# Optimization experiments

Measured on AMD Instinct MI355X. Metric: run time of the kernel, lower is better.

## Reference

```python
import jax, jax.numpy as jnp
import numpy as np
import math

B, C, H, W = 8, 64, 256, 256
E, NH = 256, 8
HD = E // NH  # 32


def get_coords(h, w):
    xx, yy = jnp.meshgrid(jnp.arange(h, dtype=jnp.float32), jnp.arange(w, dtype=jnp.float32), indexing='ij')
    return jnp.stack((xx.reshape(-1), yy.reshape(-1)), axis=-1)  # [N, 2]


def setup_inputs() -> dict:
    key = jax.random.key(0)
    ks = jax.random.split(key, 12)
    def xavier(k, shape):
        fan_out, fan_in = shape
        a = math.sqrt(6.0 / (fan_in + fan_out))
        return jax.random.uniform(k, shape, jnp.float32, -a, a)
    x = jax.random.normal(ks[0], (B, C, H, W), jnp.float32)
    z = jax.random.normal(ks[1], (B, C), jnp.float32)
    pos = jax.random.uniform(ks[2], (B, NH, 2), jnp.float32) * (H - 1)
    Wq = xavier(ks[3], (E, C)); bq = jnp.zeros((E,), jnp.float32)
    Wk = xavier(ks[4], (E, C)); bk = jnp.zeros((E,), jnp.float32)
    Wv = xavier(ks[5], (E, C)); bv = jnp.zeros((E,), jnp.float32)
    Wp = xavier(ks[6], (HD, 2)); bp = jax.random.uniform(ks[7], (HD,), jnp.float32, -1.0, 1.0) / math.sqrt(2.0)
    return {"x": x, "z": z, "pos": pos, "Wq": Wq, "bq": bq, "Wk": Wk, "bk": bk,
            "Wv": Wv, "bv": bv, "Wp": Wp, "bp": bp}


def reference(x, z, pos, Wq, bq, Wk, bk, Wv, bv, Wp, bp):
    b, c, h, w = x.shape
    n = h * w
    x_flat = x.reshape(b, c, n).transpose(0, 2, 1)          # [B, N, C]
    pos_grid = get_coords(h, w)                              # [N, 2]
    q = (z @ Wq.T + bq).reshape(b, NH, HD)                   # [B, H, hd]
    k = (x_flat @ Wk.T + bk).reshape(b, n, NH, HD)           # [B, N, H, hd]
    # relative-position modulation of keys
    rel = pos_grid[None, :, None, :] - pos[:, None, :, :]    # [B, N, H, 2]
    qxk = rel @ Wp.T + bp                                    # [B, N, H, hd]
    k = k * qxk
    v = x_flat @ Wv.T + bv                                   # [B, N, E]
    attn_logits = jnp.einsum('bhc,bnhc->bnh', q, k) / math.sqrt(HD)
    attention = jax.nn.softmax(attn_logits, axis=1)          # softmax over N
    pos_out = jnp.einsum('bnh,nx->bhx', attention, pos_grid) # [B, H, 2]
    values = jnp.einsum('bnh,bnc->bhc', attention, v)        # [B, H, E]
    return (values, pos_out)
```

## Files before the change

kernel.cpp:

```cpp
#include <hip/hip_runtime.h>

#define NN    65536
#define NSUB  128
#define NBLK  (NN/NSUB)

typedef short bf16x8 __attribute__((ext_vector_type(8)));
typedef float f32x4v __attribute__((ext_vector_type(4)));
typedef unsigned short ushort_t;
typedef unsigned int uint_t;

#define XSTR   72
#define XHI_B  0
#define XLO_B  18432
#define LGA_B  18432
#define LGSTR  28
#define PSTR   136
#define F32C_B 36864
#define RED_B  53248
#define SMEM_BYTES 53632

#define WTHI_B  0
#define WTLO_B  32768
#define CJ_B    65536
#define PM_B    66304
#define PL_B    197376
#define PSP_B   328448
#define PSX_B   590592
#define Q_B     8979200
#define QSTR    68

__device__ __forceinline__ uint_t bf16_rne_bits(float f) {
  uint_t u = __float_as_uint(f);
  return (u + 0x7FFFu + ((u >> 16) & 1u)) >> 16;
}
__device__ __forceinline__ uint_t cvt_pk_bf16(float a, float b) {
  uint_t r;
  asm("v_cvt_pk_bf16_f32 %0, %1, %2" : "=v"(r) : "v"(a), "v"(b));
  return r;
}
template <int CTRL>
__device__ __forceinline__ float dpp_add(float x) {
  int t = __builtin_amdgcn_update_dpp(0, __float_as_int(x), CTRL, 0xf, 0xf, false);
  return x + __int_as_float(t);
}
template <int CTRL>
__device__ __forceinline__ float dpp_maxs(float x) {
  int t = __builtin_amdgcn_update_dpp((int)0xFF800000u, __float_as_int(x), CTRL, 0xf, 0xf, false);
  return fmaxf(x, __int_as_float(t));
}
__device__ __forceinline__ float wave_sum(float x) {
  x = dpp_add<0x111>(x); x = dpp_add<0x112>(x); x = dpp_add<0x114>(x);
  x = dpp_add<0x118>(x); x = dpp_add<0x142>(x); x = dpp_add<0x143>(x);
  return __int_as_float(__builtin_amdgcn_readlane(__float_as_int(x), 63));
}
__device__ __forceinline__ float wave_max(float x) {
  x = dpp_maxs<0x111>(x); x = dpp_maxs<0x112>(x); x = dpp_maxs<0x114>(x);
  x = dpp_maxs<0x118>(x); x = dpp_maxs<0x142>(x); x = dpp_maxs<0x143>(x);
  return __int_as_float(__builtin_amdgcn_readlane(__float_as_int(x), 63));
}

__global__ __launch_bounds__(64) void prep_kernel(
    const float* __restrict__ z,  const float* __restrict__ Wq, const float* __restrict__ bq,
    const float* __restrict__ Wk, const float* __restrict__ bk,
    const float* __restrict__ Wp, const float* __restrict__ bp,
    ushort_t* __restrict__ WThi, ushort_t* __restrict__ WTlo, float* __restrict__ Cj)
{
  const int h = blockIdx.x, b = blockIdx.y, t = threadIdx.x;
  __shared__ float q[32];
  if (t < 32) {
    const int e = h*32 + t;
    float a = bq[e];
    const float* zr = z + b*64;
    const float* wr = Wq + e*64;
    #pragma unroll 8
    for (int c = 0; c < 64; ++c) a += zr[c]*wr[c];
    q[t] = a;
  }
  __syncthreads();
  const int c = t;
  float w[3] = {0.f, 0.f, 0.f};
  #pragma unroll 4
  for (int hd = 0; hd < 32; ++hd) {
    const float qk = q[hd] * Wk[(h*32+hd)*64 + c];
    w[0] += qk * bp[hd];
    w[1] += qk * Wp[hd*2+0];
    w[2] += qk * Wp[hd*2+1];
  }
  #pragma unroll
  for (int j = 0; j < 3; ++j) {
    const int coeff = h*3 + j;
    const uint_t hb = bf16_rne_bits(w[j]);
    const float  fh = __uint_as_float(hb << 16);
    const uint_t lb = bf16_rne_bits(w[j] - fh);
    WThi[(b*32 + coeff)*64 + c] = (ushort_t)hb;
    WTlo[(b*32 + coeff)*64 + c] = (ushort_t)lb;
  }
  if (h == 0) {
    #pragma unroll
    for (int r = 0; r < 8; ++r) {
      WThi[(b*32 + 24 + r)*64 + c] = 0;
      WTlo[(b*32 + 24 + r)*64 + c] = 0;
    }
  }
  if (t < 3) {
    float s = 0.f;
    for (int hd = 0; hd < 32; ++hd) {
      const float m = (t == 0) ? bp[hd] : Wp[hd*2 + (t-1)];
      s += q[hd] * m * bk[h*32+hd];
    }
    Cj[b*24 + h*3 + t] = s;
  }
}

#define ISSUE_CHUNK(CI)                                                              \
  do {                                                                               \
    _Pragma("unroll")                                                                \
    for (int k = 0; k < 2; ++k) {                                                    \
      const int p  = wid*2 + k;                                                      \
      const int ch = (CI)*16 + 2*p + (lid >> 5);                                     \
      const float* gsrc = xbb + (size_t)ch*NN + (lid & 31)*4;                        \
      char* ldst = smc + F32C_B + ((CI)&1)*8192 + p*1024;                            \
      __builtin_amdgcn_global_load_lds(                                              \
          (const __attribute__((address_space(1))) void*)gsrc,                       \
          (__attribute__((address_space(3))) void*)ldst, 16, 0, 0);                  \
    }                                                                                \
  } while (0)

#define CONVERT_CHUNK(CI)                                                            \
  do {                                                                               \
    const float* f32c = (const float*)(smc + F32C_B + ((CI)&1)*8192);                \
    float vv[8];                                                                     \
    _Pragma("unroll")                                                                \
    for (int j = 0; j < 8; ++j) vv[j] = f32c[(hgrp*8 + j)*128 + px];                 \
    uint_t H[4], L[4];                                                               \
    _Pragma("unroll")                                                                \
    for (int jp = 0; jp < 4; ++jp) {                                                 \
      const float f0 = vv[2*jp], f1 = vv[2*jp+1];                                    \
      const uint_t hpk = cvt_pk_bf16(f0, f1);                                        \
      const float h0 = __uint_as_float(hpk << 16);                                   \
      const float h1 = __uint_as_float(hpk & 0xFFFF0000u);                           \
      const uint_t l0 = __float_as_uint(f0 - h0);                                    \
      const uint_t l1 = __float_as_uint(f1 - h1);                                    \
      H[jp] = hpk;                                                                   \
      L[jp] = __builtin_amdgcn_perm(l1, l0, 0x07060302u);                            \
    }                                                                                \
    char* dh = smc + XHI_B + px*144 + ((CI)*2 + hgrp)*16;                            \
    char* dl = smc + XLO_B + px*144 + ((CI)*2 + hgrp)*16;                            \
    *(uint4*)dh = make_uint4(H[0], H[1], H[2], H[3]);                                \
    *(uint4*)dl = make_uint4(L[0], L[1], L[2], L[3]);                                \
  } while (0)

__global__ __launch_bounds__(256, 3) void main_kernel(
    const float* __restrict__ x, const float* __restrict__ pos,
    const ushort_t* __restrict__ WThi, const ushort_t* __restrict__ WTlo,
    const float* __restrict__ Cj,
    float* __restrict__ Pm, float* __restrict__ Pl,
    float* __restrict__ Psp, float* __restrict__ Psx)
{
  extern __shared__ char smc[];
  float*    lga = (float*)(smc + LGA_B);
  float*    red = (float*)(smc + RED_B);
  const int t   = threadIdx.x;
  const int blk = blockIdx.x;
  const int b   = blockIdx.y;
  const int n0  = blk * NSUB;
  const int wid = t >> 6, lid = t & 63;
  const int c0  = lid & 15, q4 = lid >> 4;
  const int px  = t & 127;
  const int hgrp = t >> 7;
  const int half = wid & 1;

  bf16x8 bh[2][2], bl[2][2];
  {
    const ushort_t* wtb_h = WThi + b*2048;
    const ushort_t* wtb_l = WTlo + b*2048;
    #pragma unroll
    for (int nt = 0; nt < 2; ++nt)
      #pragma unroll
      for (int ks = 0; ks < 2; ++ks) {
        const int off = (nt*16 + c0)*64 + ks*32 + q4*8;
        bh[nt][ks] = *(const bf16x8*)(wtb_h + off);
        bl[nt][ks] = *(const bf16x8*)(wtb_l + off);
      }
  }
  float cj[12];
  {
    const float* cjp = Cj + b*24 + hgrp*12;
    #pragma unroll
    for (int k = 0; k < 12; ++k) cj[k] = cjp[k];
  }
  const int gx = blk >> 1;
  float rxh[4], py[4];
  #pragma unroll
  for (int hl = 0; hl < 4; ++hl) {
    const int h = hgrp*4 + hl;
    rxh[hl] = (float)gx - pos[(b*8+h)*2 + 0];
    py[hl]  = pos[(b*8+h)*2 + 1];
  }

  const float* xbb = x + (size_t)b*64*NN + n0;
  ISSUE_CHUNK(0);
  ISSUE_CHUNK(1);

  asm volatile("s_waitcnt vmcnt(2)" ::: "memory");
  __builtin_amdgcn_sched_barrier(0);
  __builtin_amdgcn_s_barrier();
  CONVERT_CHUNK(0);
  asm volatile("s_waitcnt lgkmcnt(0)" ::: "memory");
  __builtin_amdgcn_s_barrier();
  ISSUE_CHUNK(2);

  asm volatile("s_waitcnt vmcnt(2)" ::: "memory");
  __builtin_amdgcn_sched_barrier(0);
  __builtin_amdgcn_s_barrier();
  CONVERT_CHUNK(1);
  asm volatile("s_waitcnt lgkmcnt(0)" ::: "memory");
  __builtin_amdgcn_s_barrier();
  ISSUE_CHUNK(3);

  asm volatile("s_waitcnt vmcnt(2)" ::: "memory");
  __builtin_amdgcn_sched_barrier(0);
  __builtin_amdgcn_s_barrier();
  CONVERT_CHUNK(2);

  asm volatile("s_waitcnt vmcnt(0)" ::: "memory");
  __builtin_amdgcn_sched_barrier(0);
  __builtin_amdgcn_s_barrier();
  CONVERT_CHUNK(3);

  asm volatile("s_waitcnt lgkmcnt(0)" ::: "memory");
  __builtin_amdgcn_s_barrier();

  f32x4v acc[2][2];
  #pragma unroll
  for (int mt = 0; mt < 2; ++mt) { acc[mt][0] = (f32x4v)0.f; acc[mt][1] = (f32x4v)0.f; }
  {
    const int mrow0 = wid*32;
    #pragma unroll
    for (int mt = 0; mt < 2; ++mt) {
      const int row = mrow0 + mt*16 + c0;
      const ushort_t* ph = (const ushort_t*)(smc + XHI_B) + row*XSTR + q4*8;
      const ushort_t* pl = (const ushort_t*)(smc + XLO_B) + row*XSTR + q4*8;
      bf16x8 ah0 = *(const bf16x8*)(ph);
      bf16x8 ah1 = *(const bf16x8*)(ph + 32);
      bf16x8 al0 = *(const bf16x8*)(pl);
      bf16x8 al1 = *(const bf16x8*)(pl + 32);
      #pragma unroll
      for (int nt = 0; nt < 2; ++nt) {
        f32x4v a = acc[mt][nt];
        a = __builtin_amdgcn_mfma_f32_16x16x32_bf16(ah0, bh[nt][0], a, 0, 0, 0);
        a = __builtin_amdgcn_mfma_f32_16x16x32_bf16(ah1, bh[nt][1], a, 0, 0, 0);
        a = __builtin_amdgcn_mfma_f32_16x16x32_bf16(ah0, bl[nt][0], a, 0, 0, 0);
        a = __builtin_amdgcn_mfma_f32_16x16x32_bf16(ah1, bl[nt][1], a, 0, 0, 0);
        a = __builtin_amdgcn_mfma_f32_16x16x32_bf16(al0, bh[nt][0], a, 0, 0, 0);
        a = __builtin_amdgcn_mfma_f32_16x16x32_bf16(al1, bh[nt][1], a, 0, 0, 0);
        acc[mt][nt] = a;
      }
    }
  }
  __syncthreads();

  {
    const int mrow0 = wid*32;
    #pragma unroll
    for (int mt = 0; mt < 2; ++mt)
      #pragma unroll
      for (int r = 0; r < 4; ++r) {
        const int prow = mrow0 + mt*16 + q4*4 + r;
        lga[prow*LGSTR + c0] = acc[mt][0][r];
        if (c0 < 8) lga[prow*LGSTR + 16 + c0] = acc[mt][1][r];
      }
  }
  __syncthreads();

  float a12[12];
  {
    const float4* ap = (const float4*)(lga + px*LGSTR + hgrp*12);
    #pragma unroll
    for (int r = 0; r < 3; ++r) *(float4*)(a12 + 4*r) = ap[r];
  }
  const float tf = (float)(((blk & 1) << 7) + px);
  float lg[4];
  #pragma unroll
  for (int hl = 0; hl < 4; ++hl) {
    const float a0 = a12[hl*3+0] + cj[hl*3+0];
    const float a1 = a12[hl*3+1] + cj[hl*3+1];
    const float a2 = a12[hl*3+2] + cj[hl*3+2];
    lg[hl] = (a0 + rxh[hl]*a1 + (tf - py[hl])*a2) * 0.17677669529663687f;
  }

  #pragma unroll
  for (int hl = 0; hl < 4; ++hl) {
    const float m = wave_max(lg[hl]);
    if (lid == 0) red[(hgrp*4 + hl)*2 + half] = m;
  }
  __syncthreads();

  float p[4];
  #pragma unroll
  for (int hl = 0; hl < 4; ++hl) {
    const int h = hgrp*4 + hl;
    const float M = fmaxf(red[h*2+0], red[h*2+1]);
    p[hl] = __expf(lg[hl] - M);
  }

  {
    ushort_t* pls = (ushort_t*)(smc + LGA_B);
    #pragma unroll
    for (int hl = 0; hl < 4; ++hl) {
      const int h = hgrp*4 + hl;
      const uint_t hb = bf16_rne_bits(p[hl]);
      const float  hf = __uint_as_float(hb << 16);
      const uint_t lb = __float_as_uint(p[hl] - hf) >> 16;
      pls[h*PSTR + px]       = (ushort_t)hb;
      pls[(h+8)*PSTR + px]   = (ushort_t)lb;
    }
  }

  #pragma unroll
  for (int hl = 0; hl < 4; ++hl) {
    const int h = hgrp*4 + hl;
    const float sp  = wave_sum(p[hl]);
    const float spj = wave_sum(p[hl] * tf);
    if (lid == 0) { red[16 + h*2 + half] = sp; red[32 + h*2 + half] = spj; }
  }
  __syncthreads();

  if (t < 8) {
    const int base = (b*NBLK + blk)*8 + t;
    const float M  = fmaxf(red[t*2+0], red[t*2+1]);
    const float L  = red[16+t*2+0] + red[16+t*2+1];
    const float SJ = red[32+t*2+0] + red[32+t*2+1];
    Pm[base] = M;
    Pl[base] = L;
    Psp[base*2+0] = (float)gx * L;
    Psp[base*2+1] = SJ;
  }

  {
    const ushort_t* pls = (const ushort_t*)(smc + LGA_B);
    bf16x8 afr[4];
    #pragma unroll
    for (int ks = 0; ks < 4; ++ks)
      afr[ks] = *(const bf16x8*)(pls + c0*PSTR + ks*32 + q4*8);

    f32x4v accB = (f32x4v)0.f;
    const int chbase = wid*16 + c0;
    #pragma unroll
    for (int ks = 0; ks < 4; ++ks) {
      const ushort_t* xcol = (const ushort_t*)(smc + XHI_B) + (ks*32 + q4*8)*XSTR + chbase;
      bf16x8 bfr;
      #pragma unroll
      for (int i = 0; i < 8; ++i) bfr[i] = (short)xcol[i*XSTR];
      accB = __builtin_amdgcn_mfma_f32_16x16x32_bf16(afr[ks], bfr, accB, 0, 0, 0);
    }

    const size_t pb64 = ((size_t)(b*NBLK + blk))*8*64;
    #pragma unroll
    for (int r = 0; r < 4; ++r) {
      const float o = __shfl_xor(accB[r], 32, 64);
      if (q4 < 2) {
        const int h = q4*4 + r;
        Psx[pb64 + h*64 + chbase] = accB[r] + o;
      }
    }
  }
}

__global__ __launch_bounds__(256) void reduce1_kernel(
    const float* __restrict__ Pm, const float* __restrict__ Pl,
    const float* __restrict__ Psp, const float* __restrict__ Psx,
    float* __restrict__ Q)
{
  const int g = blockIdx.x, h = blockIdx.y, b = blockIdx.z, t = threadIdx.x;
  __shared__ float al[64];
  __shared__ float mgs;
  __shared__ float sums[3];
  __shared__ float sxl[256];
  const int base = (b*NBLK + g*64)*8 + h;

  float m_t = -1e30f;
  if (t < 64) {
    m_t = Pm[base + t*8];
    float mm = m_t;
    #pragma unroll
    for (int off = 32; off >= 1; off >>= 1) mm = fmaxf(mm, __shfl_xor(mm, off, 64));
    if (t == 0) mgs = mm;
  }
  __syncthreads();
  const float Mg = mgs;
  if (t < 64) {
    const float a = __expf(m_t - Mg);
    al[t] = a;
    float lt = Pl[base + t*8] * a;
    float sx = Psp[(base + t*8)*2 + 0] * a;
    float sy = Psp[(base + t*8)*2 + 1] * a;
    #pragma unroll
    for (int off = 32; off >= 1; off >>= 1) {
      lt += __shfl_xor(lt, off, 64);
      sx += __shfl_xor(sx, off, 64);
      sy += __shfl_xor(sy, off, 64);
    }
    if (t == 0) { sums[0] = lt; sums[1] = sx; sums[2] = sy; }
  }
  __syncthreads();
  {
    const int c = t & 63, g2 = t >> 6;
    float acc = 0.f;
    #pragma unroll
    for (int i = 0; i < 16; ++i) {
      const int k = g2*16 + i;
      acc += al[k] * Psx[(size_t)(base + k*8)*64 + c];
    }
    sxl[g2*64 + c] = acc;
  }
  __syncthreads();
  float* q = Q + ((b*8 + h)*8 + g)*QSTR;
  if (t < 64) q[4+t] = sxl[t] + sxl[64+t] + sxl[128+t] + sxl[192+t];
  if (t == 0) { q[0] = Mg; q[1] = sums[0]; q[2] = sums[1]; q[3] = sums[2]; }
}

__global__ __launch_bounds__(64) void reduce2_kernel(
    const float* __restrict__ Q, const float* __restrict__ Wv, const float* __restrict__ bv,
    float* __restrict__ out)
{
  const int h = blockIdx.x, b = blockIdx.y, t = threadIdx.x;
  __shared__ float qm[8], bl[8], l8[8], sx8[8], sy8[8];
  __shared__ float SXs[64];
  const float* qb = Q + ((b*8 + h)*8)*QSTR;

  if (t < 8) qm[t] = qb[t*QSTR + 0];
  __syncthreads();
  float M = qm[0];
  #pragma unroll
  for (int g = 1; g < 8; ++g) M = fmaxf(M, qm[g]);
  if (t < 8) {
    const float be = __expf(qm[t] - M);
    bl[t]  = be;
    l8[t]  = be * qb[t*QSTR + 1];
    sx8[t] = be * qb[t*QSTR + 2];
    sy8[t] = be * qb[t*QSTR + 3];
  }
  __syncthreads();
  float L = 0.f;
  #pragma unroll
  for (int g = 0; g < 8; ++g) L += l8[g];
  const float invL = 1.0f / L;
  {
    float s = 0.f;
    #pragma unroll
    for (int g = 0; g < 8; ++g) s += bl[g] * qb[g*QSTR + 4 + t];
    SXs[t] = s * invL;
  }
  __syncthreads();

  #pragma unroll
  for (int r = 0; r < 4; ++r) {
    const int e = t + 64*r;
    float v = bv[e];
    const float* wvr = Wv + e*64;
    #pragma unroll 8
    for (int c = 0; c < 64; ++c) v += wvr[c] * SXs[c];
    out[(b*8 + h)*256 + e] = v;
  }
  if (t == 0) {
    float spx = 0.f, spy = 0.f;
    #pragma unroll
    for (int g = 0; g < 8; ++g) { spx += sx8[g]; spy += sy8[g]; }
    out[16384 + (b*8 + h)*2 + 0] = spx * invL;
    out[16384 + (b*8 + h)*2 + 1] = spy * invL;
  }
}

extern "C" void kernel_launch(void* const* d_in, const int* in_sizes, int n_in,
                              void* d_out, int out_size, void* d_ws, size_t ws_size,
                              hipStream_t stream)
{
  const float* x   = (const float*)d_in[0];
  const float* z   = (const float*)d_in[1];
  const float* pos = (const float*)d_in[2];
  const float* Wq  = (const float*)d_in[3];
  const float* bq  = (const float*)d_in[4];
  const float* Wk  = (const float*)d_in[5];
  const float* bk  = (const float*)d_in[6];
  const float* Wv  = (const float*)d_in[7];
  const float* bv  = (const float*)d_in[8];
  const float* Wp  = (const float*)d_in[9];
  const float* bp  = (const float*)d_in[10];
  float* out = (float*)d_out;
  char*  wsb = (char*)d_ws;

  ushort_t* WThi = (ushort_t*)(wsb + WTHI_B);
  ushort_t* WTlo = (ushort_t*)(wsb + WTLO_B);
  float* Cj  = (float*)(wsb + CJ_B);
  float* Pm  = (float*)(wsb + PM_B);
  float* Pl  = (float*)(wsb + PL_B);
  float* Psp = (float*)(wsb + PSP_B);
  float* Psx = (float*)(wsb + PSX_B);
  float* Q   = (float*)(wsb + Q_B);

  prep_kernel   <<<dim3(8,8),    64,  0,          stream>>>(z, Wq, bq, Wk, bk, Wp, bp, WThi, WTlo, Cj);
  main_kernel   <<<dim3(NBLK,8), 256, SMEM_BYTES, stream>>>(x, pos, WThi, WTlo, Cj, Pm, Pl, Psp, Psx);
  reduce1_kernel<<<dim3(8,8,8),  256, 0,          stream>>>(Pm, Pl, Psp, Psx, Q);
  reduce2_kernel<<<dim3(8,8),    64,  0,          stream>>>(Q, Wv, bv, out);
}
```

Measured before the change: 233.2 us.

## Make main kernel persistent with cross-tile prefetch of x chunks

The main kernel now launches a fixed grid of 96×8 blocks, each looping over pixel tiles with a stride of 96. While the last chunks of the current tile are being converted, it issues the async global-to-LDS loads for the first two chunks of its next tile. This hides load latency across tiles and removes per-block launch and prologue cost (weight fragments, Cj and pos are loaded once). The trade-off is uneven work, since 512 tiles split over 96 blocks gives 5 or 6 tiles per block, and LDS buffers are now reused across loop iterations.

```diff
diff --git a/kernel.cpp b/kernel.cpp
--- a/kernel.cpp
+++ b/kernel.cpp
@@ -3,6 +3,7 @@
 #define NN    65536
 #define NSUB  128
 #define NBLK  (NN/NSUB)
+#define GRX   96
 
 typedef short bf16x8 __attribute__((ext_vector_type(8)));
 typedef float f32x4v __attribute__((ext_vector_type(4)));
@@ -112,13 +113,13 @@
   }
 }
 
-#define ISSUE_CHUNK(CI)                                                              \
+#define ISSUE_CHUNK(CI, XPTR)                                                        \
   do {                                                                               \
     _Pragma("unroll")                                                                \
     for (int k = 0; k < 2; ++k) {                                                    \
       const int p  = wid*2 + k;                                                      \
       const int ch = (CI)*16 + 2*p + (lid >> 5);                                     \
-      const float* gsrc = xbb + (size_t)ch*NN + (lid & 31)*4;                        \
+      const float* gsrc = (XPTR) + (size_t)ch*NN + (lid & 31)*4;                     \
       char* ldst = smc + F32C_B + ((CI)&1)*8192 + p*1024;                            \
       __builtin_amdgcn_global_load_lds(                                              \
           (const __attribute__((address_space(1))) void*)gsrc,                       \
@@ -150,6 +151,18 @@
     *(uint4*)dl = make_uint4(L[0], L[1], L[2], L[3]);                                \
   } while (0)
 
+#define WAIT_VM2()                                          \
+  do { asm volatile("s_waitcnt vmcnt(2)" ::: "memory");     \
+       __builtin_amdgcn_sched_barrier(0);                   \
+       __builtin_amdgcn_s_barrier(); } while (0)
+#define WAIT_VM0()                                          \
+  do { asm volatile("s_waitcnt vmcnt(0)" ::: "memory");     \
+       __builtin_amdgcn_sched_barrier(0);                   \
+       __builtin_amdgcn_s_barrier(); } while (0)
+#define LGKM_BAR()                                          \
+  do { asm volatile("s_waitcnt lgkmcnt(0)" ::: "memory");   \
+       __builtin_amdgcn_s_barrier(); } while (0)
+
 __global__ __launch_bounds__(256, 3) void main_kernel(
     const float* __restrict__ x, const float* __restrict__ pos,
     const ushort_t* __restrict__ WThi, const ushort_t* __restrict__ WTlo,
@@ -161,9 +174,8 @@
   float*    lga = (float*)(smc + LGA_B);
   float*    red = (float*)(smc + RED_B);
   const int t   = threadIdx.x;
-  const int blk = blockIdx.x;
+  const int bx  = blockIdx.x;
   const int b   = blockIdx.y;
-  const int n0  = blk * NSUB;
   const int wid = t >> 6, lid = t & 63;
   const int c0  = lid & 15, q4 = lid >> 4;
   const int px  = t & 127;
@@ -189,179 +201,178 @@
     #pragma unroll
     for (int k = 0; k < 12; ++k) cj[k] = cjp[k];
   }
-  const int gx = blk >> 1;
-  float rxh[4], py[4];
+  float posx[4], py[4];
   #pragma unroll
   for (int hl = 0; hl < 4; ++hl) {
     const int h = hgrp*4 + hl;
-    rxh[hl] = (float)gx - pos[(b*8+h)*2 + 0];
-    py[hl]  = pos[(b*8+h)*2 + 1];
-  }
-
-  const float* xbb = x + (size_t)b*64*NN + n0;
-  ISSUE_CHUNK(0);
-  ISSUE_CHUNK(1);
-
-  asm volatile("s_waitcnt vmcnt(2)" ::: "memory");
-  __builtin_amdgcn_sched_barrier(0);
-  __builtin_amdgcn_s_barrier();
-  CONVERT_CHUNK(0);
-  asm volatile("s_waitcnt lgkmcnt(0)" ::: "memory");
-  __builtin_amdgcn_s_barrier();
-  ISSUE_CHUNK(2);
-
-  asm volatile("s_waitcnt vmcnt(2)" ::: "memory");
-  __builtin_amdgcn_sched_barrier(0);
-  __builtin_amdgcn_s_barrier();
-  CONVERT_CHUNK(1);
-  asm volatile("s_waitcnt lgkmcnt(0)" ::: "memory");
-  __builtin_amdgcn_s_barrier();
-  ISSUE_CHUNK(3);
-
-  asm volatile("s_waitcnt vmcnt(2)" ::: "memory");
-  __builtin_amdgcn_sched_barrier(0);
-  __builtin_amdgcn_s_barrier();
-  CONVERT_CHUNK(2);
-
-  asm volatile("s_waitcnt vmcnt(0)" ::: "memory");
-  __builtin_amdgcn_sched_barrier(0);
-  __builtin_amdgcn_s_barrier();
-  CONVERT_CHUNK(3);
-
-  asm volatile("s_waitcnt lgkmcnt(0)" ::: "memory");
-  __builtin_amdgcn_s_barrier();
-
-  f32x4v acc[2][2];
-  #pragma unroll
-  for (int mt = 0; mt < 2; ++mt) { acc[mt][0] = (f32x4v)0.f; acc[mt][1] = (f32x4v)0.f; }
-  {
-    const int mrow0 = wid*32;
-    #pragma unroll
-    for (int mt = 0; mt < 2; ++mt) {
-      const int row = mrow0 + mt*16 + c0;
-      const ushort_t* ph = (const ushort_t*)(smc + XHI_B) + row*XSTR + q4*8;
-      const ushort_t* pl = (const ushort_t*)(smc + XLO_B) + row*XSTR + q4*8;
-      bf16x8 ah0 = *(const bf16x8*)(ph);
-      bf16x8 ah1 = *(const bf16x8*)(ph + 32);
-      bf16x8 al0 = *(const bf16x8*)(pl);
-      bf16x8 al1 = *(const bf16x8*)(pl + 32);
-      #pragma unroll
-      for (int nt = 0; nt < 2; ++nt) {
-        f32x4v a = acc[mt][nt];
-        a = __builtin_amdgcn_mfma_f32_16x16x32_bf16(ah0, bh[nt][0], a, 0, 0, 0);
-        a = __builtin_amdgcn_mfma_f32_16x16x32_bf16(ah1, bh[nt][1], a, 0, 0, 0);
-        a = __builtin_amdgcn_mfma_f32_16x16x32_bf16(ah0, bl[nt][0], a, 0, 0, 0);
-        a = __builtin_amdgcn_mfma_f32_16x16x32_bf16(ah1, bl[nt][1], a, 0, 0, 0);
-        a = __builtin_amdgcn_mfma_f32_16x16x32_bf16(al0, bh[nt][0], a, 0, 0, 0);
-        a = __builtin_amdgcn_mfma_f32_16x16x32_bf16(al1, bh[nt][1], a, 0, 0, 0);
-        acc[mt][nt] = a;
+    posx[hl] = pos[(b*8+h)*2 + 0];
+    py[hl]   = pos[(b*8+h)*2 + 1];
+  }
+
+  const float* xb0 = x + (size_t)b*64*NN;
+
+  ISSUE_CHUNK(0, xb0 + (size_t)bx*NSUB);
+  ISSUE_CHUNK(1, xb0 + (size_t)bx*NSUB);
+
+  for (int blk = bx; blk < NBLK; blk += GRX) {
+    const bool hasn = (blk + GRX) < NBLK;
+    const float* xcur = xb0 + (size_t)blk*NSUB;
+    const float* xnxt = xb0 + (size_t)(blk + GRX)*NSUB;
+
+    WAIT_VM2();
+    CONVERT_CHUNK(0);
+    LGKM_BAR();
+    ISSUE_CHUNK(2, xcur);
+
+    WAIT_VM2();
+    CONVERT_CHUNK(1);
+    LGKM_BAR();
+    ISSUE_CHUNK(3, xcur);
+
+    WAIT_VM2();
+    CONVERT_CHUNK(2);
+    LGKM_BAR();
+    if (hasn) ISSUE_CHUNK(0, xnxt);
+
+    if (hasn) { WAIT_VM2(); }
+    else      { WAIT_VM0(); }
+    CONVERT_CHUNK(3);
+    LGKM_BAR();
+    if (hasn) ISSUE_CHUNK(1, xnxt);
+
+    f32x4v acc[2][2];
+    #pragma unroll
+    for (int mt = 0; mt < 2; ++mt) { acc[mt][0] = (f32x4v)0.f; acc[mt][1] = (f32x4v)0.f; }
+    {
+      const int mrow0 = wid*32;
+      #pragma unroll
+      for (int mt = 0; mt < 2; ++mt) {
+        const int row = mrow0 + mt*16 + c0;
+        const ushort_t* ph = (const ushort_t*)(smc + XHI_B) + row*XSTR + q4*8;
+        const ushort_t* pl = (const ushort_t*)(smc + XLO_B) + row*XSTR + q4*8;
+        bf16x8 ah0 = *(const bf16x8*)(ph);
+        bf16x8 ah1 = *(const bf16x8*)(ph + 32);
+        bf16x8 al0 = *(const bf16x8*)(pl);
+        bf16x8 al1 = *(const bf16x8*)(pl + 32);
+        #pragma unroll
+        for (int nt = 0; nt < 2; ++nt) {
+          f32x4v a = acc[mt][nt];
+          a = __builtin_amdgcn_mfma_f32_16x16x32_bf16(ah0, bh[nt][0], a, 0, 0, 0);
+          a = __builtin_amdgcn_mfma_f32_16x16x32_bf16(ah1, bh[nt][1], a, 0, 0, 0);
+          a = __builtin_amdgcn_mfma_f32_16x16x32_bf16(ah0, bl[nt][0], a, 0, 0, 0);
+          a = __builtin_amdgcn_mfma_f32_16x16x32_bf16(ah1, bl[nt][1], a, 0, 0, 0);
+          a = __builtin_amdgcn_mfma_f32_16x16x32_bf16(al0, bh[nt][0], a, 0, 0, 0);
+          a = __builtin_amdgcn_mfma_f32_16x16x32_bf16(al1, bh[nt][1], a, 0, 0, 0);
+          acc[mt][nt] = a;
+        }
       }
     }
-  }
-  __syncthreads();
-
-  {
-    const int mrow0 = wid*32;
-    #pragma unroll
-    for (int mt = 0; mt < 2; ++mt)
-      #pragma unroll
-      for (int r = 0; r < 4; ++r) {
-        const int prow = mrow0 + mt*16 + q4*4 + r;
-        lga[prow*LGSTR + c0] = acc[mt][0][r];
-        if (c0 < 8) lga[prow*LGSTR + 16 + c0] = acc[mt][1][r];
-      }
-  }
-  __syncthreads();
-
-  float a12[12];
-  {
-    const float4* ap = (const float4*)(lga + px*LGSTR + hgrp*12);
-    #pragma unroll
-    for (int r = 0; r < 3; ++r) *(float4*)(a12 + 4*r) = ap[r];
-  }
-  const float tf = (float)(((blk & 1) << 7) + px);
-  float lg[4];
-  #pragma unroll
-  for (int hl = 0; hl < 4; ++hl) {
-    const float a0 = a12[hl*3+0] + cj[hl*3+0];
-    const float a1 = a12[hl*3+1] + cj[hl*3+1];
-    const float a2 = a12[hl*3+2] + cj[hl*3+2];
-    lg[hl] = (a0 + rxh[hl]*a1 + (tf - py[hl])*a2) * 0.17677669529663687f;
-  }
-
-  #pragma unroll
-  for (int hl = 0; hl < 4; ++hl) {
-    const float m = wave_max(lg[hl]);
-    if (lid == 0) red[(hgrp*4 + hl)*2 + half] = m;
-  }
-  __syncthreads();
-
-  float p[4];
-  #pragma unroll
-  for (int hl = 0; hl < 4; ++hl) {
-    const int h = hgrp*4 + hl;
-    const float M = fmaxf(red[h*2+0], red[h*2+1]);
-    p[hl] = __expf(lg[hl] - M);
-  }
-
-  {
-    ushort_t* pls = (ushort_t*)(smc + LGA_B);
+    __syncthreads();
+
+    {
+      const int mrow0 = wid*32;
+      #pragma unroll
+      for (int mt = 0; mt < 2; ++mt)
+        #pragma unroll
+        for (int r = 0; r < 4; ++r) {
+          const int prow = mrow0 + mt*16 + q4*4 + r;
+          lga[prow*LGSTR + c0] = acc[mt][0][r];
+          if (c0 < 8) lga[prow*LGSTR + 16 + c0] = acc[mt][1][r];
+        }
+    }
+    __syncthreads();
+
+    float a12[12];
+    {
+      const float4* ap = (const float4*)(lga + px*LGSTR + hgrp*12);
+      #pragma unroll
+      for (int r = 0; r < 3; ++r) *(float4*)(a12 + 4*r) = ap[r];
+    }
+    const int   gxi = blk >> 1;
+    const float tf  = (float)(((blk & 1) << 7) + px);
+    float lg[4];
+    #pragma unroll
+    for (int hl = 0; hl < 4; ++hl) {
+      const float a0 = a12[hl*3+0] + cj[hl*3+0];
+      const float a1 = a12[hl*3+1] + cj[hl*3+1];
+      const float a2 = a12[hl*3+2] + cj[hl*3+2];
+      lg[hl] = (a0 + ((float)gxi - posx[hl])*a1 + (tf - py[hl])*a2) * 0.17677669529663687f;
+    }
+
+    #pragma unroll
+    for (int hl = 0; hl < 4; ++hl) {
+      const float m = wave_max(lg[hl]);
+      if (lid == 0) red[(hgrp*4 + hl)*2 + half] = m;
+    }
+    __syncthreads();
+
+    float p[4];
     #pragma unroll
     for (int hl = 0; hl < 4; ++hl) {
       const int h = hgrp*4 + hl;
-      const uint_t hb = bf16_rne_bits(p[hl]);
-      const float  hf = __uint_as_float(hb << 16);
-      const uint_t lb = __float_as_uint(p[hl] - hf) >> 16;
-      pls[h*PSTR + px]       = (ushort_t)hb;
-      pls[(h+8)*PSTR + px]   = (ushort_t)lb;
-    }
-  }
-
-  #pragma unroll
-  for (int hl = 0; hl < 4; ++hl) {
-    const int h = hgrp*4 + hl;
-    const float sp  = wave_sum(p[hl]);
-    const float spj = wave_sum(p[hl] * tf);
-    if (lid == 0) { red[16 + h*2 + half] = sp; red[32 + h*2 + half] = spj; }
-  }
-  __syncthreads();
-
-  if (t < 8) {
-    const int base = (b*NBLK + blk)*8 + t;
-    const float M  = fmaxf(red[t*2+0], red[t*2+1]);
-    const float L  = red[16+t*2+0] + red[16+t*2+1];
-    const float SJ = red[32+t*2+0] + red[32+t*2+1];
-    Pm[base] = M;
-    Pl[base] = L;
-    Psp[base*2+0] = (float)gx * L;
-    Psp[base*2+1] = SJ;
-  }
-
-  {
-    const ushort_t* pls = (const ushort_t*)(smc + LGA_B);
-    bf16x8 afr[4];
-    #pragma unroll
-    for (int ks = 0; ks < 4; ++ks)
-      afr[ks] = *(const bf16x8*)(pls + c0*PSTR + ks*32 + q4*8);
-
-    f32x4v accB = (f32x4v)0.f;
-    const int chbase = wid*16 + c0;
-    #pragma unroll
-    for (int ks = 0; ks < 4; ++ks) {
-      const ushort_t* xcol = (const ushort_t*)(smc + XHI_B) + (ks*32 + q4*8)*XSTR + chbase;
-      bf16x8 bfr;
-      #pragma unroll
-      for (int i = 0; i < 8; ++i) bfr[i] = (short)xcol[i*XSTR];
-      accB = __builtin_amdgcn_mfma_f32_16x16x32_bf16(afr[ks], bfr, accB, 0, 0, 0);
-    }
-
-    const size_t pb64 = ((size_t)(b*NBLK + blk))*8*64;
-    #pragma unroll
-    for (int r = 0; r < 4; ++r) {
-      const float o = __shfl_xor(accB[r], 32, 64);
-      if (q4 < 2) {
-        const int h = q4*4 + r;
-        Psx[pb64 + h*64 + chbase] = accB[r] + o;
+      const float M = fmaxf(red[h*2+0], red[h*2+1]);
+      p[hl] = __expf(lg[hl] - M);
+    }
+
+    {
+      ushort_t* pls = (ushort_t*)(smc + LGA_B);
+      #pragma unroll
+      for (int hl = 0; hl < 4; ++hl) {
+        const int h = hgrp*4 + hl;
+        const uint_t hb = bf16_rne_bits(p[hl]);
+        const float  hf = __uint_as_float(hb << 16);
+        const uint_t lb = __float_as_uint(p[hl] - hf) >> 16;
+        pls[h*PSTR + px]       = (ushort_t)hb;
+        pls[(h+8)*PSTR + px]   = (ushort_t)lb;
+      }
+    }
+
+    #pragma unroll
+    for (int hl = 0; hl < 4; ++hl) {
+      const int h = hgrp*4 + hl;
+      const float sp  = wave_sum(p[hl]);
+      const float spj = wave_sum(p[hl] * tf);
+      if (lid == 0) { red[16 + h*2 + half] = sp; red[32 + h*2 + half] = spj; }
+    }
+    __syncthreads();
+
+    if (t < 8) {
+      const int base = (b*NBLK + blk)*8 + t;
+      const float M  = fmaxf(red[t*2+0], red[t*2+1]);
+      const float L  = red[16+t*2+0] + red[16+t*2+1];
+      const float SJ = red[32+t*2+0] + red[32+t*2+1];
+      Pm[base] = M;
+      Pl[base] = L;
+      Psp[base*2+0] = (float)gxi * L;
+      Psp[base*2+1] = SJ;
+    }
+
+    {
+      const ushort_t* pls = (const ushort_t*)(smc + LGA_B);
+      bf16x8 afr[4];
+      #pragma unroll
+      for (int ks = 0; ks < 4; ++ks)
+        afr[ks] = *(const bf16x8*)(pls + c0*PSTR + ks*32 + q4*8);
+
+      f32x4v accB = (f32x4v)0.f;
+      const int chbase = wid*16 + c0;
+      #pragma unroll
+      for (int ks = 0; ks < 4; ++ks) {
+        const ushort_t* xcol = (const ushort_t*)(smc + XHI_B) + (ks*32 + q4*8)*XSTR + chbase;
+        bf16x8 bfr;
+        #pragma unroll
+        for (int i = 0; i < 8; ++i) bfr[i] = (short)xcol[i*XSTR];
+        accB = __builtin_amdgcn_mfma_f32_16x16x32_bf16(afr[ks], bfr, accB, 0, 0, 0);
+      }
+
+      const size_t pb64 = ((size_t)(b*NBLK + blk))*8*64;
+      #pragma unroll
+      for (int r = 0; r < 4; ++r) {
+        const float o = __shfl_xor(accB[r], 32, 64);
+        if (q4 < 2) {
+          const int h = q4*4 + r;
+          Psx[pb64 + h*64 + chbase] = accB[r] + o;
+        }
       }
     }
   }
@@ -499,8 +510,8 @@
   float* Psx = (float*)(wsb + PSX_B);
   float* Q   = (float*)(wsb + Q_B);
 
-  prep_kernel   <<<dim3(8,8),    64,  0,          stream>>>(z, Wq, bq, Wk, bk, Wp, bp, WThi, WTlo, Cj);
-  main_kernel   <<<dim3(NBLK,8), 256, SMEM_BYTES, stream>>>(x, pos, WThi, WTlo, Cj, Pm, Pl, Psp, Psx);
-  reduce1_kernel<<<dim3(8,8,8),  256, 0,          stream>>>(Pm, Pl, Psp, Psx, Q);
-  reduce2_kernel<<<dim3(8,8),    64,  0,          stream>>>(Q, Wv, bv, out);
-}
+  prep_kernel   <<<dim3(8,8),   64,  0,          stream>>>(z, Wq, bq, Wk, bk, Wp, bp, WThi, WTlo, Cj);
+  main_kernel   <<<dim3(GRX,8), 256, SMEM_BYTES, stream>>>(x, pos, WThi, WTlo, Cj, Pm, Pl, Psp, Psx);
+  reduce1_kernel<<<dim3(8,8,8), 256, 0,          stream>>>(Pm, Pl, Psp, Psx, Q);
+  reduce2_kernel<<<dim3(8,8),   64,  0,          stream>>>(Q, Wv, bv, out);
+}
```

New measurement: 236.4 us. About the same (+1.4%).
